# Kernel optimization log

Hardware: AMD Instinct MI355X
Metric: run time of the kernel (lower is better)

The kernel has to match this reference:

```python
import jax, jax.numpy as jnp
import numpy as np

B, T, C = 2, 2048, 2048
N_HEAD = 16

def setup_inputs() -> dict:
    key = jax.random.key(0)
    k1, k2, k3 = jax.random.split(key, 3)
    scale = 1.0 / np.sqrt(C)
    return {
        "x": jax.random.normal(k1, (B, T, C), dtype=jnp.float32),
        "w_attn": jax.random.normal(k2, (C, 3 * C), dtype=jnp.float32) * scale,
        "b_attn": jnp.zeros((3 * C,), dtype=jnp.float32),
        "w_proj": jax.random.normal(k3, (C, C), dtype=jnp.float32) * scale,
        "b_proj": jnp.zeros((C,), dtype=jnp.float32),
    }

def reference(x, w_attn, b_attn, w_proj, b_proj):
    Bb, Tt, Cc = x.shape
    hd = Cc // N_HEAD  # head_size
    qkv = x @ w_attn + b_attn              # [B,T,3C]
    q, k, v = jnp.split(qkv, 3, axis=-1)
    # [B,T,C] -> [B,H,T,hd]
    def heads(t):
        return t.reshape(Bb, Tt, N_HEAD, hd).transpose(0, 2, 1, 3)
    q, k, v = heads(q), heads(k), heads(v)
    att = jnp.einsum("bhqd,bhkd->bhqk", q, k) * (hd ** -0.5)
    causal = jnp.tril(jnp.ones((Tt, Tt), dtype=bool))
    att = jnp.where(causal[None, None], att, -jnp.inf)
    att = jax.nn.softmax(att, axis=-1)
    out = jnp.einsum("bhqk,bhkd->bhqd", att, v)
    out = out.transpose(0, 2, 1, 3).reshape(Bb, Tt, Cc)
    return out @ w_proj + b_proj
```

## Files before the change

kernel.cpp:

```cpp
#include <hip/hip_runtime.h>
#include <cstdint>
#include <cstddef>

typedef __bf16 bf16_t;
typedef __bf16 bf16x8 __attribute__((ext_vector_type(8)));
typedef __bf16 bf16x4 __attribute__((ext_vector_type(4)));
typedef float floatx4 __attribute__((ext_vector_type(4)));

#define B_  2
#define T_  2048
#define C_  2048
#define H_  16
#define HD_ 128

#define K_ATTN_SCALE (0.08838834764831843f * 1.44269504088896f)

__device__ __forceinline__ void async_copy16(const void* g, void* l) {
  __builtin_amdgcn_global_load_lds((const __attribute__((address_space(1))) unsigned int*)g,
                                   (__attribute__((address_space(3))) unsigned int*)l,
                                   16, 0, 0);
}

__global__ __launch_bounds__(256) void cvt_f32_bf16(const float* __restrict__ in,
                                                    bf16_t* __restrict__ out, int n4) {
  int i = blockIdx.x * 256 + threadIdx.x;
  if (i >= n4) return;
  const float4 v = ((const float4*)in)[i];
  bf16x4 o;
  o[0] = (bf16_t)v.x; o[1] = (bf16_t)v.y; o[2] = (bf16_t)v.z; o[3] = (bf16_t)v.w;
  ((bf16x4*)out)[i] = o;
}

__global__ __launch_bounds__(256) void transpose_cvt(const float* __restrict__ W,
                                                     bf16_t* __restrict__ Wt,
                                                     int Kd, int Nd) {
  __shared__ float tile[32][33];
  const int tx = threadIdx.x, ty = threadIdx.y;
  const int n0 = blockIdx.x * 32, k0 = blockIdx.y * 32;
#pragma unroll
  for (int j = ty; j < 32; j += 8)
    tile[j][tx] = W[(size_t)(k0 + j) * Nd + n0 + tx];
  __syncthreads();
#pragma unroll
  for (int j = ty; j < 32; j += 8)
    Wt[(size_t)(n0 + j) * Kd + k0 + tx] = (bf16_t)tile[tx][j];
}

#define TM 128
#define TN 128
#define BK 64

template <int MODE>
__global__ __launch_bounds__(256) void gemm_bt(
    const bf16_t* __restrict__ A, const bf16_t* __restrict__ Bt,
    const float* __restrict__ bias, float* __restrict__ Cout,
    bf16_t* __restrict__ Qo, bf16_t* __restrict__ Ko, bf16_t* __restrict__ Vo,
    int M, int N, int K) {
  __shared__ __align__(16) char smem[32768];
  bf16_t (*As)[BK] = (bf16_t(*)[BK])smem;
  bf16_t (*Bs)[BK] = (bf16_t(*)[BK])(smem + 16384);
  const int tid = threadIdx.x;
  const int wave = tid >> 6, lane = tid & 63;
  const int quad = lane >> 4, l15 = lane & 15;
  const int bm = blockIdx.y * TM, bn = blockIdx.x * TN;
  const int wm = (wave >> 1) * 64, wn = (wave & 1) * 64;
  const int sw = l15 & 7;

  floatx4 acc[4][4] = {};

  for (int k0 = 0; k0 < K; k0 += BK) {
#pragma unroll
    for (int it = 0; it < 4; ++it) {
      int p = it * 4096 + tid * 16;
      int r = p >> 7;
      int cg = ((p >> 4) & 7) ^ (r & 7);
      async_copy16(A + (size_t)(bm + r) * K + k0 + cg * 8, (char*)&As[0][0] + p);
      async_copy16(Bt + (size_t)(bn + r) * K + k0 + cg * 8, (char*)&Bs[0][0] + p);
    }
    __syncthreads();
#pragma unroll
    for (int kc = 0; kc < 2; ++kc) {
      const int cidx = (kc * 4 + quad) ^ sw;
      bf16x8 af[4], bf[4];
#pragma unroll
      for (int i = 0; i < 4; ++i)
        af[i] = *(const bf16x8*)&As[wm + i * 16 + l15][cidx * 8];
#pragma unroll
      for (int j = 0; j < 4; ++j)
        bf[j] = *(const bf16x8*)&Bs[wn + j * 16 + l15][cidx * 8];
#pragma unroll
      for (int i = 0; i < 4; ++i)
#pragma unroll
        for (int j = 0; j < 4; ++j)
          acc[i][j] = __builtin_amdgcn_mfma_f32_16x16x32_bf16(af[i], bf[j], acc[i][j], 0, 0, 0);
    }
    __syncthreads();
  }

  if (MODE == 0 && bn >= 2 * C_) {
    bf16_t* vt = (bf16_t*)smem;
    const int h = (bn - 2 * C_) >> 7;
    const int b = bm >> 11;
    const int t0g = bm & 2047;
#pragma unroll
    for (int i = 0; i < 4; ++i) {
#pragma unroll
      for (int j = 0; j < 4; ++j) {
#pragma unroll
        for (int r = 0; r < 4; ++r) {
          int tl = wm + i * 16 + quad * 4 + r;
          int d  = wn + j * 16 + l15;
          float val = acc[i][j][r] + bias[bn + wn + j * 16 + l15];
          vt[d * 128 + (tl ^ (8 * (d & 15)))] = (bf16_t)val;
        }
      }
    }
    __syncthreads();
    const int row = tid >> 1, half = tid & 1;
    bf16_t* dst = Vo + ((size_t)(b * H_ + h) * HD_ + row) * T_ + t0g;
#pragma unroll
    for (int cc = 0; cc < 8; ++cc) {
      int c = half * 8 + cc;
      uint4 v = *(const uint4*)&vt[row * 128 + ((c ^ (row & 15)) * 8)];
      *(uint4*)(dst + c * 8) = v;
    }
    return;
  }

#pragma unroll
  for (int i = 0; i < 4; ++i) {
#pragma unroll
    for (int j = 0; j < 4; ++j) {
#pragma unroll
      for (int r = 0; r < 4; ++r) {
        int m = bm + wm + i * 16 + quad * 4 + r;
        int n = bn + wn + j * 16 + l15;
        float val = acc[i][j][r] + bias[n];
        if (MODE == 1) {
          Cout[(size_t)m * N + n] = val;
        } else {
          int which = n >> 11;
          int cc = n & 2047;
          int h = cc >> 7, d = cc & 127;
          int b = m >> 11, t = m & 2047;
          if (which == 0) val *= K_ATTN_SCALE;
          bf16_t bv = (bf16_t)val;
          bf16_t* dst = (which == 0) ? Qo : Ko;
          dst[(((size_t)(b * H_ + h)) * T_ + t) * HD_ + d] = bv;
        }
      }
    }
  }
}

__global__ __launch_bounds__(256) void attn(const bf16_t* __restrict__ Q,
                                            const bf16_t* __restrict__ Kg,
                                            const bf16_t* __restrict__ Vt,
                                            bf16_t* __restrict__ O) {
  __shared__ bf16_t Ks[2][64][128];
  __shared__ bf16_t Vs[2][128][64];
  const int tid = threadIdx.x;
  const int wave = tid >> 6, lane = tid & 63;
  const int quad = lane >> 4, l15 = lane & 15;
  const int j = blockIdx.x;
  const int bh = blockIdx.y;
  const int b = bh >> 4, h = bh & 15;
  const int qtA = 31 - j, qtB = j;
  const int nchA = qtA + 1, nchB = qtB + 1;
  const int q0A = qtA * 64 + wave * 16;
  const int q0B = qtB * 64 + wave * 16;

  const bf16_t* Qh = Q + (size_t)bh * T_ * HD_;
  const bf16_t* Kh = Kg + (size_t)bh * T_ * HD_;
  const bf16_t* Vh = Vt + (size_t)bh * HD_ * T_;

  bf16x8 qfA[4], qfB[4];
#pragma unroll
  for (int kk = 0; kk < 4; ++kk) {
    qfA[kk] = *(const bf16x8*)(Qh + (size_t)(q0A + l15) * HD_ + kk * 32 + quad * 8);
    qfB[kk] = *(const bf16x8*)(Qh + (size_t)(q0B + l15) * HD_ + kk * 32 + quad * 8);
  }

  floatx4 oaccA[8] = {}, oaccB[8] = {};
  float l_A = 0.0f, l_B = 0.0f;

  union PU { bf16x4 v; long long u; };
  union PF { long long u[2]; bf16x8 v; };
  const int lo = ((lane & 16) << 1) + l15;

  auto stage = [&](int buf, int kt0) {
#pragma unroll
    for (int it = 0; it < 4; ++it) {
      int p = it * 4096 + tid * 16;
      int r = p >> 8;
      int cg = ((p >> 4) & 15) ^ (r & 15);
      async_copy16(Kh + (size_t)(kt0 + r) * HD_ + cg * 8, (char*)&Ks[buf][0][0] + p);
    }
#pragma unroll
    for (int it = 0; it < 4; ++it) {
      int p = it * 4096 + tid * 16;
      int r = p >> 7;
      int cg = ((p >> 4) & 7) ^ (r & 7);
      async_copy16(Vh + (size_t)r * T_ + kt0 + cg * 8, (char*)&Vs[buf][0][0] + p);
    }
  };

  auto step = [&](int buf, const bf16x8* qf, floatx4* oacc, float& l_i, int q0, int kt0,
                  bool mask) {
    floatx4 s[4] = {{}, {}, {}, {}};
#pragma unroll
    for (int st = 0; st < 4; ++st) {
#pragma unroll
      for (int kk = 0; kk < 4; ++kk) {
        bf16x8 kf = *(const bf16x8*)&Ks[buf][st * 16 + l15][(((kk * 4 + quad) ^ l15) & 15) * 8];
        s[st] = __builtin_amdgcn_mfma_f32_16x16x32_bf16(kf, qf[kk], s[st], 0, 0, 0);
      }
    }
    float ps = 0.0f;
    long long pu[4];
#pragma unroll
    for (int st = 0; st < 4; ++st) {
      PU t;
#pragma unroll
      for (int r = 0; r < 4; ++r) {
        float val = s[st][r];
        if (mask) {
          int kt = kt0 + st * 16 + quad * 4 + r;
          val = (kt <= q0 + l15) ? val : -3.0e38f;
        }
        float p = exp2f(val);
        ps += p;
        t.v[r] = (bf16_t)p;
      }
      pu[st] = t.u;
    }
    ps += __shfl_xor(ps, 16);
    ps += __shfl_xor(ps, 32);
    l_i += ps;
#pragma unroll
    for (int bb = 0; bb < 2; ++bb) {
      long long lo0 = __shfl(pu[2 * bb], lo);
      long long hi0 = __shfl(pu[2 * bb], lo + 16);
      long long lo1 = __shfl(pu[2 * bb + 1], lo);
      long long hi1 = __shfl(pu[2 * bb + 1], lo + 16);
      PF pf;
      pf.u[0] = (quad >= 2) ? lo1 : lo0;
      pf.u[1] = (quad >= 2) ? hi1 : hi0;
#pragma unroll
      for (int dt = 0; dt < 8; ++dt) {
        bf16x8 vf = *(const bf16x8*)&Vs[buf][dt * 16 + l15][(((bb * 4 + quad) ^ l15) & 7) * 8];
        oacc[dt] = __builtin_amdgcn_mfma_f32_16x16x32_bf16(pf.v, vf, oacc[dt], 0, 0, 0);
      }
    }
  };

  stage(0, 0);
  for (int ch = 0; ch < nchA; ++ch) {
    __syncthreads();
    if (ch + 1 < nchA) stage((ch + 1) & 1, (ch + 1) * 64);
    const int kt0 = ch * 64;
    const int buf = ch & 1;
    step(buf, qfA, oaccA, l_A, q0A, kt0, ch == nchA - 1);
    if (ch < nchB) step(buf, qfB, oaccB, l_B, q0B, kt0, ch == nchB - 1);
  }

  float lrA[4], lrB[4];
#pragma unroll
  for (int r = 0; r < 4; ++r) {
    lrA[r] = __shfl(l_A, quad * 4 + r);
    lrB[r] = __shfl(l_B, quad * 4 + r);
  }
#pragma unroll
  for (int dt = 0; dt < 8; ++dt) {
#pragma unroll
    for (int r = 0; r < 4; ++r) {
      int d = dt * 16 + l15;
      int qa = q0A + quad * 4 + r;
      int qb = q0B + quad * 4 + r;
      O[((size_t)(b * T_ + qa)) * C_ + h * HD_ + d] = (bf16_t)(oaccA[dt][r] / lrA[r]);
      O[((size_t)(b * T_ + qb)) * C_ + h * HD_ + d] = (bf16_t)(oaccB[dt][r] / lrB[r]);
    }
  }
}

extern "C" void kernel_launch(void* const* d_in, const int* in_sizes, int n_in,
                              void* d_out, int out_size, void* d_ws, size_t ws_size,
                              hipStream_t stream) {
  const float* x      = (const float*)d_in[0];
  const float* w_attn = (const float*)d_in[1];
  const float* b_attn = (const float*)d_in[2];
  const float* w_proj = (const float*)d_in[3];
  const float* b_proj = (const float*)d_in[4];
  float* out = (float*)d_out;

  char* p = (char*)d_ws;
  bf16_t* xb  = (bf16_t*)p; p += (size_t)4096 * 2048 * 2;
  bf16_t* waT = (bf16_t*)p; p += (size_t)6144 * 2048 * 2;
  bf16_t* wpT = (bf16_t*)p; p += (size_t)2048 * 2048 * 2;
  bf16_t* Qb  = (bf16_t*)p; p += (size_t)32 * 2048 * 128 * 2;
  bf16_t* Kb  = (bf16_t*)p; p += (size_t)32 * 2048 * 128 * 2;
  bf16_t* Vb  = (bf16_t*)p; p += (size_t)32 * 2048 * 128 * 2;
  bf16_t* Ob  = (bf16_t*)p; p += (size_t)4096 * 2048 * 2;

  cvt_f32_bf16<<<8192, 256, 0, stream>>>(x, xb, 2097152);
  transpose_cvt<<<dim3(6144 / 32, 2048 / 32), dim3(32, 8), 0, stream>>>(w_attn, waT, 2048, 6144);
  transpose_cvt<<<dim3(2048 / 32, 2048 / 32), dim3(32, 8), 0, stream>>>(w_proj, wpT, 2048, 2048);

  gemm_bt<0><<<dim3(6144 / TN, 4096 / TM), 256, 0, stream>>>(
      xb, waT, b_attn, nullptr, Qb, Kb, Vb, 4096, 6144, 2048);

  attn<<<dim3(16, 32), 256, 0, stream>>>(Qb, Kb, Vb, Ob);

  gemm_bt<1><<<dim3(2048 / TN, 4096 / TM), 256, 0, stream>>>(
      Ob, wpT, b_proj, out, nullptr, nullptr, nullptr, 4096, 2048, 2048);
}
```

Before: 421.5 us.

## Replace QKV GEMM with 256x256-tiled double-buffered async-LDS kernel

```diff
diff --git a/kernel.cpp b/kernel.cpp
--- a/kernel.cpp
+++ b/kernel.cpp
@@ -46,15 +46,158 @@
     Wt[(size_t)(n0 + j) * Kd + k0 + tx] = (bf16_t)tile[tx][j];
 }
 
+#define GBM 256
+#define GBN 256
+#define GBK 64
+
+__global__ __launch_bounds__(512, 2) void gemm_qkv(
+    const bf16_t* __restrict__ A, const bf16_t* __restrict__ Bt,
+    const float* __restrict__ bias,
+    bf16_t* __restrict__ Qo, bf16_t* __restrict__ Ko, bf16_t* __restrict__ Vo,
+    int K) {
+  __shared__ __align__(16) char smem[131072];
+  const int tid = threadIdx.x;
+  const int wave = tid >> 6, lane = tid & 63;
+  const int quad = lane >> 4, l15 = lane & 15;
+  const int wm = wave >> 2, wn = wave & 3;
+  const int bm = blockIdx.y * GBM, bn = blockIdx.x * GBN;
+
+  const bf16_t* asrc[4];
+  const bf16_t* bsrc[4];
+#pragma unroll
+  for (int l = 0; l < 4; ++l) {
+    int p = l * 8192 + tid * 16;
+    int q = p ^ (((p >> 9) & 1) << 5) ^ (((p >> 10) & 1) << 4);
+    int r = q >> 7, c8 = (q >> 4) & 7;
+    asrc[l] = A  + (size_t)(bm + r) * K + c8 * 8;
+    bsrc[l] = Bt + (size_t)(bn + r) * K + c8 * 8;
+  }
+
+  auto stage = [&](int buf, int k0) {
+    char* As = smem + buf * 65536;
+    char* Bs = As + 32768;
+#pragma unroll
+    for (int l = 0; l < 4; ++l) {
+      int p = l * 8192 + tid * 16;
+      async_copy16(asrc[l] + k0, As + p);
+      async_copy16(bsrc[l] + k0, Bs + p);
+    }
+  };
+
+  const int sx = ((l15 & 4) << 3) | ((l15 & 8) << 1);
+  const int cq = quad * 16;
+  const int arow = (wm * 128 + l15) << 7;
+  const int brow = (wn * 64 + l15) << 7;
+
+  floatx4 acc[8][4] = {};
+
+  stage(0, 0);
+  asm volatile("s_waitcnt vmcnt(0)" ::: "memory");
+  __builtin_amdgcn_s_barrier();
+
+  const int NT = K / GBK;
+  for (int t = 0; t < NT; ++t) {
+    const int buf = t & 1;
+    const char* As = smem + buf * 65536;
+    const char* Bs = As + 32768;
+    if (t + 1 < NT) stage(buf ^ 1, (t + 1) * GBK);
+
+#pragma unroll
+    for (int mq = 0; mq < 2; ++mq) {
+      bf16x8 af[4][2];
+#pragma unroll
+      for (int i = 0; i < 4; ++i)
+#pragma unroll
+        for (int ks = 0; ks < 2; ++ks)
+          af[i][ks] = *(const bf16x8*)(As + arow + (((mq * 64 + i * 16)) << 7) +
+                                       ((ks * 64 + cq) ^ sx));
+#pragma unroll
+      for (int nq = 0; nq < 2; ++nq) {
+        bf16x8 bfr[2][2];
+#pragma unroll
+        for (int j = 0; j < 2; ++j)
+#pragma unroll
+          for (int ks = 0; ks < 2; ++ks)
+            bfr[j][ks] = *(const bf16x8*)(Bs + brow + (((nq * 32 + j * 16)) << 7) +
+                                          ((ks * 64 + cq) ^ sx));
+        __builtin_amdgcn_s_barrier();
+        __builtin_amdgcn_s_setprio(1);
+#pragma unroll
+        for (int i = 0; i < 4; ++i)
+#pragma unroll
+          for (int j = 0; j < 2; ++j)
+#pragma unroll
+            for (int ks = 0; ks < 2; ++ks)
+              acc[mq * 4 + i][nq * 2 + j] = __builtin_amdgcn_mfma_f32_16x16x32_bf16(
+                  af[i][ks], bfr[j][ks], acc[mq * 4 + i][nq * 2 + j], 0, 0, 0);
+        __builtin_amdgcn_s_setprio(0);
+        if (mq == 1 && nq == 1)
+          asm volatile("s_waitcnt vmcnt(0)" ::: "memory");
+        __builtin_amdgcn_s_barrier();
+      }
+    }
+  }
+
+  float bias_r[4];
+#pragma unroll
+  for (int jj = 0; jj < 4; ++jj)
+    bias_r[jj] = bias[bn + wn * 64 + (jj >> 1) * 32 + (jj & 1) * 16 + l15];
+
+  if (bn < 2 * C_) {
+    const int which = bn >> 11;
+    bf16_t* dst0 = which ? Ko : Qo;
+    const float scl = which ? 1.0f : K_ATTN_SCALE;
+#pragma unroll
+    for (int ii = 0; ii < 8; ++ii) {
+      const int m = bm + wm * 128 + (ii >> 2) * 64 + (ii & 3) * 16 + quad * 4;
+      const int b = m >> 11, tq = m & 2047;
+#pragma unroll
+      for (int jj = 0; jj < 4; ++jj) {
+        const int n = bn + wn * 64 + (jj >> 1) * 32 + (jj & 1) * 16 + l15;
+        const int cc = n & 2047;
+        const int h = cc >> 7, d = cc & 127;
+        bf16_t* dst = dst0 + (((size_t)(b * H_ + h)) * T_ + tq) * HD_ + d;
+#pragma unroll
+        for (int r = 0; r < 4; ++r)
+          dst[(size_t)r * HD_] = (bf16_t)((acc[ii][jj][r] + bias_r[jj]) * scl);
+      }
+    }
+  } else {
+    __syncthreads();
+    bf16_t* vt = (bf16_t*)smem;
+#pragma unroll
+    for (int ii = 0; ii < 8; ++ii) {
+      const int tl = wm * 128 + (ii >> 2) * 64 + (ii & 3) * 16 + quad * 4;
+#pragma unroll
+      for (int jj = 0; jj < 4; ++jj) {
+        const int dl = wn * 64 + (jj >> 1) * 32 + (jj & 1) * 16 + l15;
+        const int sw = 8 * (dl & 15);
+#pragma unroll
+        for (int r = 0; r < 4; ++r)
+          vt[dl * 256 + ((tl + r) ^ sw)] = (bf16_t)(acc[ii][jj][r] + bias_r[jj]);
+      }
+    }
+    __syncthreads();
+    const int dr = tid >> 1, half = tid & 1;
+    const int h = ((bn - 2 * C_) >> 7) + (dr >> 7);
+    const int b = bm >> 11, t0g = bm & 2047;
+    bf16_t* dst = Vo + ((size_t)(b * H_ + h) * HD_ + (dr & 127)) * T_ + t0g;
+#pragma unroll
+    for (int cc2 = 0; cc2 < 16; ++cc2) {
+      const int c = half * 16 + cc2;
+      uint4 v = *(const uint4*)&vt[dr * 256 + ((c ^ (dr & 15)) * 8)];
+      *(uint4*)(dst + c * 8) = v;
+    }
+  }
+}
+
 #define TM 128
 #define TN 128
 #define BK 64
 
-template <int MODE>
-__global__ __launch_bounds__(256) void gemm_bt(
+__global__ __launch_bounds__(256) void gemm_proj(
     const bf16_t* __restrict__ A, const bf16_t* __restrict__ Bt,
     const float* __restrict__ bias, float* __restrict__ Cout,
-    bf16_t* __restrict__ Qo, bf16_t* __restrict__ Ko, bf16_t* __restrict__ Vo,
     int M, int N, int K) {
   __shared__ __align__(16) char smem[32768];
   bf16_t (*As)[BK] = (bf16_t(*)[BK])smem;
@@ -97,36 +240,6 @@
     __syncthreads();
   }
 
-  if (MODE == 0 && bn >= 2 * C_) {
-    bf16_t* vt = (bf16_t*)smem;
-    const int h = (bn - 2 * C_) >> 7;
-    const int b = bm >> 11;
-    const int t0g = bm & 2047;
-#pragma unroll
-    for (int i = 0; i < 4; ++i) {
-#pragma unroll
-      for (int j = 0; j < 4; ++j) {
-#pragma unroll
-        for (int r = 0; r < 4; ++r) {
-          int tl = wm + i * 16 + quad * 4 + r;
-          int d  = wn + j * 16 + l15;
-          float val = acc[i][j][r] + bias[bn + wn + j * 16 + l15];
-          vt[d * 128 + (tl ^ (8 * (d & 15)))] = (bf16_t)val;
-        }
-      }
-    }
-    __syncthreads();
-    const int row = tid >> 1, half = tid & 1;
-    bf16_t* dst = Vo + ((size_t)(b * H_ + h) * HD_ + row) * T_ + t0g;
-#pragma unroll
-    for (int cc = 0; cc < 8; ++cc) {
-      int c = half * 8 + cc;
-      uint4 v = *(const uint4*)&vt[row * 128 + ((c ^ (row & 15)) * 8)];
-      *(uint4*)(dst + c * 8) = v;
-    }
-    return;
-  }
-
 #pragma unroll
   for (int i = 0; i < 4; ++i) {
 #pragma unroll
@@ -135,19 +248,7 @@
       for (int r = 0; r < 4; ++r) {
         int m = bm + wm + i * 16 + quad * 4 + r;
         int n = bn + wn + j * 16 + l15;
-        float val = acc[i][j][r] + bias[n];
-        if (MODE == 1) {
-          Cout[(size_t)m * N + n] = val;
-        } else {
-          int which = n >> 11;
-          int cc = n & 2047;
-          int h = cc >> 7, d = cc & 127;
-          int b = m >> 11, t = m & 2047;
-          if (which == 0) val *= K_ATTN_SCALE;
-          bf16_t bv = (bf16_t)val;
-          bf16_t* dst = (which == 0) ? Qo : Ko;
-          dst[(((size_t)(b * H_ + h)) * T_ + t) * HD_ + d] = bv;
-        }
+        Cout[(size_t)m * N + n] = acc[i][j][r] + bias[n];
       }
     }
   }
@@ -306,11 +407,11 @@
   transpose_cvt<<<dim3(6144 / 32, 2048 / 32), dim3(32, 8), 0, stream>>>(w_attn, waT, 2048, 6144);
   transpose_cvt<<<dim3(2048 / 32, 2048 / 32), dim3(32, 8), 0, stream>>>(w_proj, wpT, 2048, 2048);
 
-  gemm_bt<0><<<dim3(6144 / TN, 4096 / TM), 256, 0, stream>>>(
-      xb, waT, b_attn, nullptr, Qb, Kb, Vb, 4096, 6144, 2048);
+  gemm_qkv<<<dim3(6144 / GBN, 4096 / GBM), 512, 0, stream>>>(
+      xb, waT, b_attn, Qb, Kb, Vb, 2048);
 
   attn<<<dim3(16, 32), 256, 0, stream>>>(Qb, Kb, Vb, Ob);
 
-  gemm_bt<1><<<dim3(2048 / TN, 4096 / TM), 256, 0, stream>>>(
-      Ob, wpT, b_proj, out, nullptr, nullptr, nullptr, 4096, 2048, 2048);
-}
+  gemm_proj<<<dim3(2048 / TN, 4096 / TM), 256, 0, stream>>>(
+      Ob, wpT, b_proj, out, 4096, 2048, 2048);
+}
```

New measurement: 484.9 us. +15.1%, slower.
